# Optimization experiments

Measured on AMD Instinct MI355X. Metric: run time of the kernel, lower is better.

Reference implementation:

```python
import jax, jax.numpy as jnp
import numpy as np

B, TK, NK, H = 64, 512, 256, 512

def _masked_renorm_softmax(scores, mask):
    # softmax over last dim, multiply by mask, renormalize (as in the torch code)
    p = jax.nn.softmax(scores, axis=-1) * mask
    return p / jnp.sum(p, axis=-1, keepdims=True)

def setup_inputs() -> dict:
    key = jax.random.key(0)
    ks = jax.random.split(key, 14)
    s = 0.02
    return {
        "s_t_hat": jax.random.normal(ks[0], (B, 2 * H), jnp.float32),
        "encoder_outputs_token": jax.random.normal(ks[1], (B, TK, H), jnp.float32),
        "encoder_outputs_node": jax.random.normal(ks[2], (B, NK, H), jnp.float32),
        "node_to_token": jax.random.randint(ks[3], (B, TK), 0, NK),
        "enc_padding_mask_token": jnp.ones((B, TK), jnp.float32),
        "enc_padding_mask_node": jnp.ones((B, NK), jnp.float32),
        "graph": jax.random.uniform(ks[4], (B, NK, NK), jnp.float32),
        "flow": jax.random.uniform(ks[5], (B, NK), jnp.float32),
        # parameters (Linear weights stored as [in, out]; x @ W == torch Linear)
        "W_c": jax.random.normal(ks[6], (H,), jnp.float32) * s,          # Linear(1, H)
        "W_tok": jax.random.normal(ks[7], (H, H), jnp.float32) * s,      # encode_proj_token
        "W_node": jax.random.normal(ks[8], (H, H), jnp.float32) * s,     # encode_proj_node
        "W_dec": jax.random.normal(ks[9], (2 * H, H), jnp.float32) * s,  # decode_proj
        "b_dec": jnp.zeros((H,), jnp.float32),
        "v_tok": jax.random.normal(ks[10], (H,), jnp.float32) * s,       # v_token
        "v_node": jax.random.normal(ks[11], (H,), jnp.float32) * s,      # v_node
    }

def reference(s_t_hat, encoder_outputs_token, encoder_outputs_node, node_to_token,
              enc_padding_mask_token, enc_padding_mask_node, graph, flow,
              W_c, W_tok, W_node, W_dec, b_dec, v_tok, v_node):
    # projections
    enc_tok_feat = jnp.einsum('bth,hk->btk', encoder_outputs_token, W_tok)   # [B,TK,H]
    enc_node_feat = jnp.einsum('bnh,hk->bnk', encoder_outputs_node, W_node)  # [B,NK,H]
    dec_fea = s_t_hat @ W_dec + b_dec                                        # [B,H]
    flow_feat = flow[..., None] * W_c                                        # [B,NK,H]

    # node attention
    e_node = jnp.tanh(enc_node_feat + dec_fea[:, None, :] + flow_feat)
    scores_node = jnp.einsum('bnh,h->bn', e_node, v_node)                    # [B,NK]
    attn_dist_node = _masked_renorm_softmax(scores_node, enc_padding_mask_node)

    # gather node attention onto tokens via node_to_token indices
    gathered = jnp.take_along_axis(attn_dist_node, node_to_token, axis=1)    # [B,TK]
    attn_dist_node_to_token = _masked_renorm_softmax(gathered, enc_padding_mask_token)

    # token attention
    e_tok = jnp.tanh(enc_tok_feat + dec_fea[:, None, :])
    scores_tok = jnp.einsum('bth,h->bt', e_tok, v_tok)                       # [B,TK]
    attn_dist_token = _masked_renorm_softmax(scores_tok, enc_padding_mask_token)

    # mix and context
    final_attn = 0.5 * attn_dist_token + 0.5 * attn_dist_node_to_token      # [B,TK]
    c_t = jnp.einsum('bt,bth->bh', final_attn, encoder_outputs_token)        # [B,H]

    # multi-hop graph diffusion of node attention
    zero_hop = attn_dist_node                                                # [B,NK]
    one_hop = jnp.einsum('bn,bnm->bm', zero_hop, graph)
    two_hop = jnp.einsum('bn,bnm->bm', one_hop, graph)
    flow_out = (zero_hop + one_hop + two_hop) * 0.33333

    return (c_t, final_attn, attn_dist_node, flow_out)
```

## Files before the change

### kernel.cpp

```cpp
#include <hip/hip_runtime.h>
#include <math.h>

constexpr int kB = 64;
constexpr int kTK = 512;
constexpr int kNK = 256;
constexpr int kH = 512;
constexpr int kTokBlocks = kB * kTK / 64;
constexpr int kNodeBlocks = kB * kNK / 64;

typedef float f32x4 __attribute__((ext_vector_type(4)));
typedef __bf16 bf16x8 __attribute__((ext_vector_type(8)));

__device__ __forceinline__ unsigned short f32_to_bf16(float f) {
  return (unsigned short)((__float_as_uint(f) + 0x8000u) >> 16);
}

__device__ __forceinline__ float tanh_fast(float x) {
  float e = __builtin_amdgcn_exp2f(x * 2.8853900817779268f);
  return 1.0f - 2.0f * __builtin_amdgcn_rcpf(e + 1.0f);
}

__device__ __forceinline__ void lds_barrier() {
  __builtin_amdgcn_s_waitcnt(0xC07F);
  __builtin_amdgcn_s_barrier();
}

__global__ __launch_bounds__(256) void prep_kernel(
    const float* __restrict__ Wtok, const float* __restrict__ Wnode,
    unsigned short* __restrict__ WtokT, unsigned short* __restrict__ WnodeT,
    const float* __restrict__ s_t_hat, const float* __restrict__ W_dec,
    float* __restrict__ dec_part) {
  __shared__ float sm[32 * 33];
  const int tid = threadIdx.x;
  if (blockIdx.x < 512) {
    const int idx = blockIdx.x;
    const int z = idx >> 8, rem = idx & 255;
    const int bx = rem & 15, by = rem >> 4;
    const float* W = z ? Wnode : Wtok;
    unsigned short* T = z ? WnodeT : WtokT;
    const int tx = tid & 31, ty = tid >> 5;
#pragma unroll
    for (int i = 0; i < 4; ++i)
      sm[(ty + 8 * i) * 33 + tx] =
          W[(size_t)(by * 32 + ty + 8 * i) * kH + bx * 32 + tx];
    __syncthreads();
#pragma unroll
    for (int i = 0; i < 4; ++i)
      T[(size_t)(bx * 32 + ty + 8 * i) * kH + by * 32 + tx] =
          f32_to_bf16(sm[tx * 33 + ty + 8 * i]);
  } else {
    const int r = blockIdx.x - 512;
    const int b = r >> 3, s = r & 7;
    if (tid < 128) sm[tid] = s_t_hat[(size_t)b * 1024 + s * 128 + tid];
    __syncthreads();
    float a0 = 0.f, a1 = 0.f;
    const float* w = W_dec + (size_t)(s * 128) * kH;
#pragma unroll 8
    for (int k = 0; k < 128; ++k) {
      a0 = fmaf(sm[k], w[(size_t)k * kH + tid], a0);
      a1 = fmaf(sm[k], w[(size_t)k * kH + tid + 256], a1);
    }
    dec_part[(size_t)(b * 8 + s) * kH + tid] = a0;
    dec_part[(size_t)(b * 8 + s) * kH + tid + 256] = a1;
  }
}

__global__ __launch_bounds__(1024, 4) void scores_fused_kernel(
    const float* __restrict__ enc_tok, const float* __restrict__ enc_node,
    const unsigned short* __restrict__ WtokT,
    const unsigned short* __restrict__ WnodeT,
    const float* __restrict__ dec_part, const float* __restrict__ b_dec,
    const float* __restrict__ flow, const float* __restrict__ W_c,
    const float* __restrict__ v_tok, const float* __restrict__ v_node,
    float* __restrict__ scores_tok, float* __restrict__ scores_node) {
  const int tid = threadIdx.x;
  const int wave = tid >> 6, lane = tid & 63;
  const int quad = lane >> 4, l15 = lane & 15;
  const bool is_node = blockIdx.x >= kTokBlocks;
  const int bidx = is_node ? (int)blockIdx.x - kTokBlocks : (int)blockIdx.x;
  const float* A = is_node ? enc_node : enc_tok;
  const unsigned short* WT = is_node ? WnodeT : WtokT;
  const float* v = is_node ? v_node : v_tok;
  float* scores = is_node ? scores_node : scores_tok;
  const int ROWS = is_node ? kNK : kTK;
  const int b = is_node ? (bidx >> 2) : (bidx >> 3);
  const int row0 = (is_node ? (bidx & 3) : (bidx & 7)) * 64;

  __shared__ __align__(16) unsigned short As[2][8192];
  __shared__ float red[16][64];

  const f32x4 fzero = {0.f, 0.f, 0.f, 0.f};
  f32x4 acc[4][2];
#pragma unroll
  for (int i = 0; i < 4; ++i)
#pragma unroll
    for (int j = 0; j < 2; ++j) acc[i][j] = fzero;

  const int r = tid >> 4;
  const int kcol = tid & 15;
  const float* aptr = A + (size_t)(b * ROWS + row0 + r) * kH + kcol * 4;
  const int k0 = kcol * 4;
  const int k1 = 64 + kcol * 4;
  const int addr0 = (((k0 >> 5) * 4 + (r >> 4)) * 64 + ((k0 >> 3) & 3) * 16 +
                     (r & 15)) * 8 + (k0 & 7);
  const int addr1 = (((k1 >> 5) * 4 + (r >> 4)) * 64 + ((k1 >> 3) & 3) * 16 +
                     (r & 15)) * 8 + (k1 & 7);
  float4 ax0, ax1;
  auto aload = [&](int kc) {
    ax0 = *(const float4*)(aptr + kc * 128);
    ax1 = *(const float4*)(aptr + kc * 128 + 64);
  };
  auto acommit = [&](int buf) {
    ushort4 h0, h1;
    h0.x = f32_to_bf16(ax0.x); h0.y = f32_to_bf16(ax0.y);
    h0.z = f32_to_bf16(ax0.z); h0.w = f32_to_bf16(ax0.w);
    h1.x = f32_to_bf16(ax1.x); h1.y = f32_to_bf16(ax1.y);
    h1.z = f32_to_bf16(ax1.z); h1.w = f32_to_bf16(ax1.w);
    *(ushort4*)&As[buf][addr0] = h0;
    *(ushort4*)&As[buf][addr1] = h1;
  };

  const int n0 = wave * 32;
  const unsigned short* bbase = WT + (size_t)(n0 + l15) * kH + quad * 8;
  bf16x8 bbuf[2][2];
  auto loadB = [&](int sb, int g) {
    bbuf[sb][0] = *(const bf16x8*)(bbase + g * 32);
    bbuf[sb][1] = *(const bf16x8*)(bbase + (size_t)16 * kH + g * 32);
  };

  aload(0);
  acommit(0);
  aload(1);
  loadB(0, 0);
  lds_barrier();

#pragma unroll
  for (int g = 0; g < 16; ++g) {
    const int kc = g >> 2, kh = g & 3;
    if (kh == 0 && kc < 3) {
      acommit((kc + 1) & 1);
      if (kc < 2) aload(kc + 2);
    }
    if (g < 15) loadB((g + 1) & 1, g + 1);
    bf16x8 afr[4];
#pragma unroll
    for (int mi = 0; mi < 4; ++mi)
      afr[mi] = *(const bf16x8*)&As[kc & 1][((kh * 4 + mi) * 64 + lane) * 8];
#pragma unroll
    for (int mi = 0; mi < 4; ++mi)
#pragma unroll
      for (int ni = 0; ni < 2; ++ni)
        acc[mi][ni] = __builtin_amdgcn_mfma_f32_16x16x32_bf16(
            afr[mi], bbuf[g & 1][ni], acc[mi][ni], 0, 0, 0);
    if (kh == 3 && kc < 3) lds_barrier();
  }

  float dec2[2], vv2[2], wc2[2];
#pragma unroll
  for (int ni = 0; ni < 2; ++ni) {
    const int col = n0 + 16 * ni + l15;
    float d = b_dec[col];
#pragma unroll
    for (int p = 0; p < 8; ++p) d += dec_part[(size_t)(b * 8 + p) * kH + col];
    dec2[ni] = d;
    vv2[ni] = v[col];
    wc2[ni] = is_node ? W_c[col] : 0.f;
  }
#pragma unroll
  for (int mi = 0; mi < 4; ++mi) {
#pragma unroll
    for (int reg = 0; reg < 4; ++reg) {
      const int row = 16 * mi + quad * 4 + reg;
      const float fl = is_node ? flow[b * kNK + row0 + row] : 0.f;
      float p = 0.f;
#pragma unroll
      for (int ni = 0; ni < 2; ++ni)
        p += tanh_fast(fmaf(fl, wc2[ni], acc[mi][ni][reg] + dec2[ni])) * vv2[ni];
#pragma unroll
      for (int off = 1; off < 16; off <<= 1) p += __shfl_xor(p, off, 64);
      if (l15 == 0) red[wave][row] = p;
    }
  }
  __syncthreads();
  if (tid < 64) {
    float s = 0.f;
#pragma unroll
    for (int w = 0; w < 16; ++w) s += red[w][tid];
    scores[b * ROWS + row0 + tid] = s;
  }
}

__device__ __forceinline__ float block_sum_512(float v, float* rbuf) {
#pragma unroll
  for (int off = 32; off >= 1; off >>= 1) v += __shfl_xor(v, off, 64);
  if ((threadIdx.x & 63) == 0) rbuf[threadIdx.x >> 6] = v;
  __syncthreads();
  float s = rbuf[0];
#pragma unroll
  for (int w = 1; w < 8; ++w) s += rbuf[w];
  __syncthreads();
  return s;
}

__global__ __launch_bounds__(512) void softmax_mix_kernel(
    const float* __restrict__ scores_node, const float* __restrict__ scores_tok,
    const int* __restrict__ node_to_token,
    const float* __restrict__ mask_tok, const float* __restrict__ mask_node,
    float* __restrict__ out_final, float* __restrict__ out_attn_node,
    float* __restrict__ out_flow) {
  const int b = blockIdx.x, tid = threadIdx.x;
  __shared__ float an_sh[kNK];
  __shared__ float rbuf[8];

  if (tid < kNK) out_flow[b * kNK + tid] = 0.f;

  float en = 0.f;
  if (tid < kNK)
    en = expf(scores_node[b * kNK + tid]) * mask_node[b * kNK + tid];
  float sn = block_sum_512(en, rbuf);
  float an = en / sn;
  if (tid < kNK) {
    an_sh[tid] = an;
    out_attn_node[b * kNK + tid] = an;
  }
  __syncthreads();

  const float mt = mask_tok[b * kTK + tid];
  const int idx = node_to_token[b * kTK + tid];
  float eg = expf(an_sh[idx]) * mt;
  float sg = block_sum_512(eg, rbuf);
  float an2t = eg / sg;

  float et = expf(scores_tok[b * kTK + tid]) * mt;
  float st = block_sum_512(et, rbuf);
  float at = et / st;

  out_final[b * kTK + tid] = 0.5f * (at + an2t);
}

__global__ __launch_bounds__(512) void ct_flow1_kernel(
    const float* __restrict__ final_attn, const float* __restrict__ enc_tok,
    const float* __restrict__ attn_node, const float* __restrict__ graph,
    float* __restrict__ ctp, float* __restrict__ fp1) {
  const int tid = threadIdx.x;
  if (blockIdx.x < 128) {
    const int b = blockIdx.x >> 1, s = blockIdx.x & 1;
    __shared__ float fa[256];
    if (tid < 256) fa[tid] = final_attn[b * kTK + s * 256 + tid];
    __syncthreads();
    const int h4 = (tid & 127) * 4, tsub = tid >> 7;
    float4 acc = {0.f, 0.f, 0.f, 0.f};
    const float* base =
        enc_tok + ((size_t)(b * kTK + s * 256 + tsub * 64)) * kH + h4;
#pragma unroll 8
    for (int t = 0; t < 64; ++t) {
      float4 e = *(const float4*)(base + (size_t)t * kH);
      const float w = fa[tsub * 64 + t];
      acc.x = fmaf(w, e.x, acc.x); acc.y = fmaf(w, e.y, acc.y);
      acc.z = fmaf(w, e.z, acc.z); acc.w = fmaf(w, e.w, acc.w);
    }
    *(float4*)&ctp[((size_t)(b * 8 + s * 4 + tsub)) * kH + h4] = acc;
  } else {
    const int rr = blockIdx.x - 128;
    const int b = rr >> 2, sl = rr & 3;
    __shared__ float z[64];
    __shared__ float part[8][256];
    if (tid < 64) z[tid] = attn_node[b * kNK + sl * 64 + tid];
    __syncthreads();
    const int m4 = (tid & 63) * 4, nsub = tid >> 6;
    float4 acc = {0.f, 0.f, 0.f, 0.f};
    const float* g =
        graph + ((size_t)(b * kNK + sl * 64 + nsub * 8)) * kNK + m4;
#pragma unroll
    for (int n = 0; n < 8; ++n) {
      float4 gg = *(const float4*)(g + (size_t)n * kNK);
      const float w = z[nsub * 8 + n];
      acc.x = fmaf(w, gg.x, acc.x); acc.y = fmaf(w, gg.y, acc.y);
      acc.z = fmaf(w, gg.z, acc.z); acc.w = fmaf(w, gg.w, acc.w);
    }
    *(float4*)&part[nsub][m4] = acc;
    __syncthreads();
    if (tid < 64) {
      float4 s0 = {0.f, 0.f, 0.f, 0.f};
#pragma unroll
      for (int p = 0; p < 8; ++p) {
        float4 pp = *(const float4*)&part[p][tid * 4];
        s0.x += pp.x; s0.y += pp.y; s0.z += pp.z; s0.w += pp.w;
      }
      *(float4*)&fp1[((size_t)(b * 4 + sl)) * kNK + tid * 4] = s0;
    }
  }
}

__global__ __launch_bounds__(512) void ct_flow2_kernel(
    const float* __restrict__ ctp, const float* __restrict__ fp1,
    const float* __restrict__ attn_node, const float* __restrict__ graph,
    float* __restrict__ out_ct, float* __restrict__ out_flow) {
  const int tid = threadIdx.x;
  if (blockIdx.x < 64) {
    const int b = blockIdx.x;
    __shared__ float acc_sh[4][512];
    const int h4 = (tid & 127) * 4, part = tid >> 7;
    float4 a = {0.f, 0.f, 0.f, 0.f};
#pragma unroll
    for (int j = 0; j < 2; ++j) {
      float4 c = *(const float4*)&ctp[((size_t)(b * 8 + part * 2 + j)) * kH + h4];
      a.x += c.x; a.y += c.y; a.z += c.z; a.w += c.w;
    }
    *(float4*)&acc_sh[part][h4] = a;
    __syncthreads();
    if (tid < 128) {
      float4 s = {0.f, 0.f, 0.f, 0.f};
#pragma unroll
      for (int p = 0; p < 4; ++p) {
        float4 pp = *(const float4*)&acc_sh[p][tid * 4];
        s.x += pp.x; s.y += pp.y; s.z += pp.z; s.w += pp.w;
      }
      *(float4*)&out_ct[b * kH + tid * 4] = s;
    }
  } else {
    const int rr = blockIdx.x - 64;
    const int b = rr >> 2, sl = rr & 3;
    __shared__ float one_sh[64];
    __shared__ float part2[8][256];
    if (tid < 64) {
      const int n = sl * 64 + tid;
      float one = 0.f;
#pragma unroll
      for (int p = 0; p < 4; ++p) one += fp1[((size_t)(b * 4 + p)) * kNK + n];
      one_sh[tid] = one;
      atomicAdd(&out_flow[b * kNK + n],
                (attn_node[b * kNK + n] + one) * 0.33333f);
    }
    __syncthreads();
    const int m4 = (tid & 63) * 4, nsub = tid >> 6;
    float4 acc = {0.f, 0.f, 0.f, 0.f};
    const float* g =
        graph + ((size_t)(b * kNK + sl * 64 + nsub * 8)) * kNK + m4;
#pragma unroll
    for (int n = 0; n < 8; ++n) {
      float4 gg = *(const float4*)(g + (size_t)n * kNK);
      const float w = one_sh[sl * 0 + nsub * 8 + n];
      acc.x = fmaf(w, gg.x, acc.x); acc.y = fmaf(w, gg.y, acc.y);
      acc.z = fmaf(w, gg.z, acc.z); acc.w = fmaf(w, gg.w, acc.w);
    }
    *(float4*)&part2[nsub][m4] = acc;
    __syncthreads();
    if (tid < 64) {
      float4 s = {0.f, 0.f, 0.f, 0.f};
#pragma unroll
      for (int p = 0; p < 8; ++p) {
        float4 pp = *(const float4*)&part2[p][tid * 4];
        s.x += pp.x; s.y += pp.y; s.z += pp.z; s.w += pp.w;
      }
      float* dst = &out_flow[b * kNK + tid * 4];
      atomicAdd(dst + 0, s.x * 0.33333f);
      atomicAdd(dst + 1, s.y * 0.33333f);
      atomicAdd(dst + 2, s.z * 0.33333f);
      atomicAdd(dst + 3, s.w * 0.33333f);
    }
  }
}

extern "C" void kernel_launch(void* const* d_in, const int* in_sizes, int n_in,
                              void* d_out, int out_size, void* d_ws, size_t ws_size,
                              hipStream_t stream) {
  (void)in_sizes; (void)n_in; (void)out_size; (void)ws_size;
  const float* s_t_hat  = (const float*)d_in[0];
  const float* enc_tok  = (const float*)d_in[1];
  const float* enc_node = (const float*)d_in[2];
  const int*   n2t      = (const int*)d_in[3];
  const float* mask_tok = (const float*)d_in[4];
  const float* mask_nd  = (const float*)d_in[5];
  const float* graph    = (const float*)d_in[6];
  const float* flow     = (const float*)d_in[7];
  const float* W_c      = (const float*)d_in[8];
  const float* W_tok    = (const float*)d_in[9];
  const float* W_node   = (const float*)d_in[10];
  const float* W_dec    = (const float*)d_in[11];
  const float* b_dec    = (const float*)d_in[12];
  const float* v_tok    = (const float*)d_in[13];
  const float* v_node   = (const float*)d_in[14];

  float* out = (float*)d_out;
  float* out_ct        = out;
  float* out_final     = out + kB * kH;
  float* out_attn_node = out + 2 * kB * kH;
  float* out_flow      = out_attn_node + kB * kNK;

  float* ws = (float*)d_ws;
  float* scores_tok  = ws;
  float* scores_node = ws + 32768;
  float* dec_part    = ws + 49152;
  float* ctp         = dec_part;
  float* fp1         = ws + 311296;
  unsigned short* WtokT  = (unsigned short*)(ws + 376832);
  unsigned short* WnodeT = WtokT + kH * kH;

  prep_kernel<<<1024, 256, 0, stream>>>(W_tok, W_node, WtokT, WnodeT,
                                        s_t_hat, W_dec, dec_part);
  scores_fused_kernel<<<kTokBlocks + kNodeBlocks, 1024, 0, stream>>>(
      enc_tok, enc_node, WtokT, WnodeT, dec_part, b_dec, flow, W_c,
      v_tok, v_node, scores_tok, scores_node);
  softmax_mix_kernel<<<kB, 512, 0, stream>>>(scores_node, scores_tok, n2t,
                                             mask_tok, mask_nd, out_final,
                                             out_attn_node, out_flow);
  ct_flow1_kernel<<<384, 512, 0, stream>>>(out_final, enc_tok, out_attn_node,
                                           graph, ctp, fp1);
  ct_flow2_kernel<<<320, 512, 0, stream>>>(ctp, fp1, out_attn_node, graph,
                                           out_ct, out_flow);
}
```

Baseline: 240.6 us.

## Swizzle LDS tile, deepen A/B prefetch, and split context reduction across more blocks

The fused scores GEMM now XOR-swizzles the bf16 A tile in shared memory to cut bank conflicts. It uses two register sets for A prefetch so global loads run further ahead, and holds four B register buffers for a three-step-ahead prefetch. The context-vector part of ct_flow1 moves from 128 to 512 blocks, each covering 64 tokens and reducing its four partials in shared memory before writing one partial row, which gives more parallelism on that bandwidth-bound pass. The cost is higher register pressure in the GEMM and an extra shared-memory reduction plus barrier in the context kernel.

```diff
diff --git a/kernel.cpp b/kernel.cpp
--- a/kernel.cpp
+++ b/kernel.cpp
@@ -101,57 +101,68 @@
   const float* aptr = A + (size_t)(b * ROWS + row0 + r) * kH + kcol * 4;
   const int k0 = kcol * 4;
   const int k1 = 64 + kcol * 4;
-  const int addr0 = (((k0 >> 5) * 4 + (r >> 4)) * 64 + ((k0 >> 3) & 3) * 16 +
-                     (r & 15)) * 8 + (k0 & 7);
-  const int addr1 = (((k1 >> 5) * 4 + (r >> 4)) * 64 + ((k1 >> 3) & 3) * 16 +
-                     (r & 15)) * 8 + (k1 & 7);
-  float4 ax0, ax1;
-  auto aload = [&](int kc) {
-    ax0 = *(const float4*)(aptr + kc * 128);
-    ax1 = *(const float4*)(aptr + kc * 128 + 64);
+  const int s0 = ((k0 >> 5) * 4 + (r >> 4)) * 64 + ((k0 >> 3) & 3) * 16 + (r & 15);
+  const int s1 = ((k1 >> 5) * 4 + (r >> 4)) * 64 + ((k1 >> 3) & 3) * 16 + (r & 15);
+  const int sw0 = s0 ^ (((s0 >> 4) & 3) << 1) ^ ((s0 >> 8) & 1);
+  const int sw1 = s1 ^ (((s1 >> 4) & 3) << 1) ^ ((s1 >> 8) & 1);
+  const int addr0 = sw0 * 8 + (k0 & 7);
+  const int addr1 = sw1 * 8 + (k1 & 7);
+
+  float4 axA0, axA1, axB0, axB1;
+  auto aloadA = [&](int kc) {
+    axA0 = *(const float4*)(aptr + kc * 128);
+    axA1 = *(const float4*)(aptr + kc * 128 + 64);
   };
-  auto acommit = [&](int buf) {
+  auto aloadB = [&](int kc) {
+    axB0 = *(const float4*)(aptr + kc * 128);
+    axB1 = *(const float4*)(aptr + kc * 128 + 64);
+  };
+  auto commit = [&](int buf, float4 x0, float4 x1) {
     ushort4 h0, h1;
-    h0.x = f32_to_bf16(ax0.x); h0.y = f32_to_bf16(ax0.y);
-    h0.z = f32_to_bf16(ax0.z); h0.w = f32_to_bf16(ax0.w);
-    h1.x = f32_to_bf16(ax1.x); h1.y = f32_to_bf16(ax1.y);
-    h1.z = f32_to_bf16(ax1.z); h1.w = f32_to_bf16(ax1.w);
+    h0.x = f32_to_bf16(x0.x); h0.y = f32_to_bf16(x0.y);
+    h0.z = f32_to_bf16(x0.z); h0.w = f32_to_bf16(x0.w);
+    h1.x = f32_to_bf16(x1.x); h1.y = f32_to_bf16(x1.y);
+    h1.z = f32_to_bf16(x1.z); h1.w = f32_to_bf16(x1.w);
     *(ushort4*)&As[buf][addr0] = h0;
     *(ushort4*)&As[buf][addr1] = h1;
   };
 
   const int n0 = wave * 32;
   const unsigned short* bbase = WT + (size_t)(n0 + l15) * kH + quad * 8;
-  bf16x8 bbuf[2][2];
+  bf16x8 bbuf[4][2];
   auto loadB = [&](int sb, int g) {
     bbuf[sb][0] = *(const bf16x8*)(bbase + g * 32);
     bbuf[sb][1] = *(const bf16x8*)(bbase + (size_t)16 * kH + g * 32);
   };
 
-  aload(0);
-  acommit(0);
-  aload(1);
+  aloadA(0);
+  aloadB(1);
   loadB(0, 0);
+  loadB(1, 1);
+  loadB(2, 2);
+  commit(0, axA0, axA1);
+  aloadA(2);
   lds_barrier();
 
 #pragma unroll
   for (int g = 0; g < 16; ++g) {
     const int kc = g >> 2, kh = g & 3;
-    if (kh == 0 && kc < 3) {
-      acommit((kc + 1) & 1);
-      if (kc < 2) aload(kc + 2);
-    }
-    if (g < 15) loadB((g + 1) & 1, g + 1);
+    if (g == 0) { commit(1, axB0, axB1); aloadB(3); }
+    else if (g == 4) { commit(0, axA0, axA1); }
+    else if (g == 8) { commit(1, axB0, axB1); }
+    if (g < 13) loadB((g + 3) & 3, g + 3);
     bf16x8 afr[4];
 #pragma unroll
-    for (int mi = 0; mi < 4; ++mi)
-      afr[mi] = *(const bf16x8*)&As[kc & 1][((kh * 4 + mi) * 64 + lane) * 8];
+    for (int mi = 0; mi < 4; ++mi) {
+      const int slot = ((kh * 4 + mi) * 64 + lane) ^ (((lane >> 4) & 3) << 1) ^ (kh & 1);
+      afr[mi] = *(const bf16x8*)&As[kc & 1][slot * 8];
+    }
 #pragma unroll
     for (int mi = 0; mi < 4; ++mi)
 #pragma unroll
       for (int ni = 0; ni < 2; ++ni)
         acc[mi][ni] = __builtin_amdgcn_mfma_f32_16x16x32_bf16(
-            afr[mi], bbuf[g & 1][ni], acc[mi][ni], 0, 0, 0);
+            afr[mi], bbuf[g & 3][ni], acc[mi][ni], 0, 0, 0);
     if (kh == 3 && kc < 3) lds_barrier();
   }
 
@@ -243,25 +254,36 @@
     const float* __restrict__ attn_node, const float* __restrict__ graph,
     float* __restrict__ ctp, float* __restrict__ fp1) {
   const int tid = threadIdx.x;
-  if (blockIdx.x < 128) {
-    const int b = blockIdx.x >> 1, s = blockIdx.x & 1;
-    __shared__ float fa[256];
-    if (tid < 256) fa[tid] = final_attn[b * kTK + s * 256 + tid];
+  if (blockIdx.x < 512) {
+    const int b = blockIdx.x >> 3, s = blockIdx.x & 7;
+    __shared__ float fa[64];
+    __shared__ float part[4][512];
+    if (tid < 64) fa[tid] = final_attn[b * kTK + s * 64 + tid];
     __syncthreads();
     const int h4 = (tid & 127) * 4, tsub = tid >> 7;
     float4 acc = {0.f, 0.f, 0.f, 0.f};
     const float* base =
-        enc_tok + ((size_t)(b * kTK + s * 256 + tsub * 64)) * kH + h4;
-#pragma unroll 8
-    for (int t = 0; t < 64; ++t) {
+        enc_tok + ((size_t)(b * kTK + s * 64 + tsub * 16)) * kH + h4;
+#pragma unroll
+    for (int t = 0; t < 16; ++t) {
       float4 e = *(const float4*)(base + (size_t)t * kH);
-      const float w = fa[tsub * 64 + t];
+      const float w = fa[tsub * 16 + t];
       acc.x = fmaf(w, e.x, acc.x); acc.y = fmaf(w, e.y, acc.y);
       acc.z = fmaf(w, e.z, acc.z); acc.w = fmaf(w, e.w, acc.w);
     }
-    *(float4*)&ctp[((size_t)(b * 8 + s * 4 + tsub)) * kH + h4] = acc;
+    *(float4*)&part[tsub][h4] = acc;
+    __syncthreads();
+    if (tid < 128) {
+      float4 s0 = {0.f, 0.f, 0.f, 0.f};
+#pragma unroll
+      for (int p = 0; p < 4; ++p) {
+        float4 pp = *(const float4*)&part[p][tid * 4];
+        s0.x += pp.x; s0.y += pp.y; s0.z += pp.z; s0.w += pp.w;
+      }
+      *(float4*)&ctp[((size_t)(b * 8 + s)) * kH + tid * 4] = s0;
+    }
   } else {
-    const int rr = blockIdx.x - 128;
+    const int rr = blockIdx.x - 512;
     const int b = rr >> 2, sl = rr & 3;
     __shared__ float z[64];
     __shared__ float part[8][256];
@@ -405,7 +427,7 @@
   softmax_mix_kernel<<<kB, 512, 0, stream>>>(scores_node, scores_tok, n2t,
                                              mask_tok, mask_nd, out_final,
                                              out_attn_node, out_flow);
-  ct_flow1_kernel<<<384, 512, 0, stream>>>(out_final, enc_tok, out_attn_node,
+  ct_flow1_kernel<<<768, 512, 0, stream>>>(out_final, enc_tok, out_attn_node,
                                            graph, ctp, fp1);
   ct_flow2_kernel<<<320, 512, 0, stream>>>(ctp, fp1, out_attn_node, graph,
                                            out_ct, out_flow);
```

After: 241.9 us. About the same (+0.5%).
